# Kernel tuning notes

Measured on AMD Instinct MI355X. Metric: run time of the kernel, lower is better.

The kernel has to match this reference:

```python
import jax, jax.numpy as jnp
import numpy as np

E, T, D, H = 32, 65536, 512, 1024


def setup_inputs() -> dict:
    key = jax.random.key(0)
    k = jax.random.split(key, 7)
    norm = lambda kk, shp, sc: (jax.random.normal(kk, shp, jnp.float32) * sc)
    x = norm(k[0], (T, D), 1.0)
    w1 = norm(k[1], (E, D, H), D ** -0.5)   # per-expert up-proj (gate branch)
    b1 = norm(k[2], (E, H), 0.02)
    w3 = norm(k[3], (E, D, H), D ** -0.5)   # per-expert up-proj (linear branch)
    b3 = norm(k[4], (E, H), 0.02)
    w2 = norm(k[5], (E, H, D), H ** -0.5)   # per-expert down-proj
    b2 = norm(k[6], (E, D), 0.02)
    # tokens are pre-sorted by expert; uniform dispatch of T//E tokens per expert
    group_sizes = jnp.full((E,), T // E, jnp.int32)
    return dict(x=x, w1=w1, b1=b1, w3=w3, b3=b3, w2=w2, b2=b2,
                group_sizes=group_sizes)


def reference(x, w1, b1, w3, b3, w2, b2, group_sizes):
    # expert id per token, derived from contiguous group sizes
    bounds = jnp.cumsum(group_sizes)                       # [E]
    seg = jnp.searchsorted(bounds, jnp.arange(x.shape[0]), side='right')  # [T]
    # grouped GEMMs: per-expert weight bank applied to its contiguous token slab
    h1 = jax.lax.ragged_dot(x, w1, group_sizes) + b1[seg]  # [T,H]
    h3 = jax.lax.ragged_dot(x, w3, group_sizes) + b3[seg]  # [T,H]
    h = jax.nn.silu(h1) * h3                               # SwiGLU gate
    out = jax.lax.ragged_dot(h, w2, group_sizes) + b2[seg] # [T,D]
    return out
```

## Files before the change

kernel.cpp:

```cpp
#include <hip/hip_runtime.h>
#include <hip/hip_bf16.h>

#define TOK 65536
#define NE  32
#define DD  512
#define HH  1024
#define TPE 2048

typedef short s16x8  __attribute__((ext_vector_type(8)));
typedef float f32x16 __attribute__((ext_vector_type(16)));
using u16 = unsigned short;
using u32 = unsigned int;

__device__ __forceinline__ u16 f2bf(float f) {
  __bf16 h = (__bf16)f;
  return __builtin_bit_cast(u16, h);
}
__device__ __forceinline__ u32 pk2(float lo, float hi) {
  return (u32)f2bf(lo) | ((u32)f2bf(hi) << 16);
}
__device__ __forceinline__ int swz(int row, int colb) {
  return (row << 7) + (colb ^ ((row & 7) << 4));
}

#define MFMA(a, b, c) __builtin_amdgcn_mfma_f32_32x32x16_bf16(a, b, c, 0, 0, 0)
#define GLD(src, dst) __builtin_amdgcn_global_load_lds( \
    (const __attribute__((address_space(1))) void*)(src), \
    (__attribute__((address_space(3))) void*)(dst), 16, 0, 0)
#define SETP(n) __builtin_amdgcn_s_setprio(n)
#define SCHEDB() __builtin_amdgcn_sched_barrier(0)
#define SBAR()  __builtin_amdgcn_s_barrier()

__global__ __launch_bounds__(256) void p1_cvt_x(
    const float* __restrict__ x, u16* __restrict__ xb) {
  const size_t i = ((size_t)blockIdx.x * 256 + threadIdx.x) * 8;
  const float4 a = *(const float4*)(x + i);
  const float4 b = *(const float4*)(x + i + 4);
  uint4 v;
  v.x = pk2(a.x, a.y); v.y = pk2(a.z, a.w);
  v.z = pk2(b.x, b.y); v.w = pk2(b.z, b.w);
  *(uint4*)(xb + i) = v;
}

__global__ __launch_bounds__(256) void p2_w13t(
    const float* __restrict__ w1, const float* __restrict__ w3,
    u16* __restrict__ w13t) {
  __shared__ __align__(16) u16 L1[64 * 72], L3[64 * 72];
  const int bid = blockIdx.x;
  const int e = bid >> 7, rr = bid & 127;
  const int d0 = (rr & 7) << 6, h0 = (rr >> 3) << 6;
  const int t = threadIdx.x;
  const float* const s1 = w1 + (size_t)e * DD * HH + (size_t)d0 * HH + h0;
  const float* const s3 = w3 + (size_t)e * DD * HH + (size_t)d0 * HH + h0;
  const int cg = (t & 15) << 2, rbase = t >> 4;
#pragma unroll
  for (int j = 0; j < 4; ++j) {
    const int dr = rbase + (j << 4);
    const float4 a = *(const float4*)(s1 + (size_t)dr * HH + cg);
    const float4 b = *(const float4*)(s3 + (size_t)dr * HH + cg);
    L1[(cg + 0) * 72 + dr] = f2bf(a.x); L1[(cg + 1) * 72 + dr] = f2bf(a.y);
    L1[(cg + 2) * 72 + dr] = f2bf(a.z); L1[(cg + 3) * 72 + dr] = f2bf(a.w);
    L3[(cg + 0) * 72 + dr] = f2bf(b.x); L3[(cg + 1) * 72 + dr] = f2bf(b.y);
    L3[(cg + 2) * 72 + dr] = f2bf(b.z); L3[(cg + 3) * 72 + dr] = f2bf(b.w);
  }
  __syncthreads();
  u16* const dst = w13t + (size_t)e * (2 * HH) * DD;
  const int cb8 = (t & 7) << 3;
#pragma unroll
  for (int j = 0; j < 2; ++j) {
    const int nloc = (t >> 3) + (j << 5);
    const int n = h0 + nloc;
    const int R1 = ((n >> 5) << 6) + (n & 31);
    const uint4 v1 = *(const uint4*)(L1 + nloc * 72 + cb8);
    const uint4 v3 = *(const uint4*)(L3 + nloc * 72 + cb8);
    *(uint4*)(dst + (size_t)R1 * DD + d0 + cb8) = v1;
    *(uint4*)(dst + (size_t)(R1 + 32) * DD + d0 + cb8) = v3;
  }
}

__global__ __launch_bounds__(256) void p3_w2t(
    const float* __restrict__ w2, u16* __restrict__ w2t) {
  __shared__ __align__(16) u16 L[64 * 72];
  const int bid = blockIdx.x;
  const int e = bid >> 7, rr = bid & 127;
  const int d0 = (rr & 7) << 6, h0 = (rr >> 3) << 6;
  const int t = threadIdx.x;
  const float* const s = w2 + (size_t)e * HH * DD + (size_t)h0 * DD + d0;
  const int cg = (t & 15) << 2, rbase = t >> 4;
#pragma unroll
  for (int j = 0; j < 4; ++j) {
    const int hr = rbase + (j << 4);
    const float4 a = *(const float4*)(s + (size_t)hr * DD + cg);
    L[(cg + 0) * 72 + hr] = f2bf(a.x); L[(cg + 1) * 72 + hr] = f2bf(a.y);
    L[(cg + 2) * 72 + hr] = f2bf(a.z); L[(cg + 3) * 72 + hr] = f2bf(a.w);
  }
  __syncthreads();
  u16* const dst = w2t + (size_t)e * DD * HH;
  const int cb8 = (t & 7) << 3;
#pragma unroll
  for (int j = 0; j < 2; ++j) {
    const int dloc = (t >> 3) + (j << 5);
    const uint4 v = *(const uint4*)(L + dloc * 72 + cb8);
    *(uint4*)(dst + (size_t)(d0 + dloc) * HH + h0 + cb8) = v;
  }
}

template <int MODE>
__global__ __launch_bounds__(512, 2) void gemm4p(
    const u16* __restrict__ A, const u16* __restrict__ Bm,
    const float* __restrict__ bx, const float* __restrict__ by,
    void* __restrict__ outp) {
  constexpr int K  = MODE ? HH : DD;
  constexpr int NT = K >> 6;
  constexpr int NB = MODE ? 2 : 8;
  constexpr int NWG = NE * 8 * NB;
  __shared__ __align__(16) char lds[131072];

  int bid = blockIdx.x;
  bid = (bid & 7) * (NWG / 8) + (bid >> 3);
  const int e   = bid / (8 * NB);
  const int rr  = bid % (8 * NB);
  const int m_t = rr & 7;
  const int n_t = rr >> 3;
  const int rowbase = e * TPE + (m_t << 8);

  const int t = threadIdx.x;
  const int wv = t >> 6, lane = t & 63;
  const int l31 = lane & 31, half = lane >> 5;
  const int wm = wv >> 2, wn = wv & 3;

  const u16* const Abase = A + (size_t)rowbase * K;
  const u16* const Bbase = Bm + ((size_t)e * NB + n_t) * 256 * K;

  int srcoff0, srcoff1;
  {
    const int c0 = t,       lr0 = c0 >> 3, s0 = (c0 & 7) ^ (lr0 & 7);
    const int c1 = 512 + t, lr1 = c1 >> 3, s1 = (c1 & 7) ^ (lr1 & 7);
    srcoff0 = ((lr0 << 1) | (s0 >> 2)) * K + ((s0 & 3) << 3);
    srcoff1 = ((lr1 << 1) | (s1 >> 2)) * K + ((s1 & 3) << 3);
  }
  const int t16 = t << 4;

  auto stageQ = [&](int tau, int q) {
    const u16* const src = ((q & 1) ? Bbase : Abase) + tau * 64 + (q >> 1) * 32;
    char* const dst = lds + ((tau & 1) << 16) + (q << 14);
    GLD(src + srcoff0, dst + t16);
    GLD(src + srcoff1, dst + 8192 + t16);
  };

  const int lrow_off = l31 >> 1;
  const int pbit = l31 & 1;
  const int sw7 = lrow_off & 7;
  const int sA0 = (((pbit << 2) | 0 | half) ^ sw7) << 4;
  const int sA1 = (((pbit << 2) | 2 | half) ^ sw7) << 4;
  const int aoff = ((wm << 6) + lrow_off) << 7;
  const int boff = ((wn << 5) + lrow_off) << 7;

  f32x16 acc[4][2] = {};
  s16x8 b00{}, b01{}, b10{}, b11{};

#define VM6 asm volatile("s_waitcnt vmcnt(6)" ::: "memory")
#define VM4 asm volatile("s_waitcnt vmcnt(4)" ::: "memory")
#define VM0 asm volatile("s_waitcnt vmcnt(0)" ::: "memory")
#define NOPV ((void)0)

#define PHASE(T, KH, MH, DOB, STG, VM) do { \
  STG; VM; \
  SCHEDB(); SBAR(); SCHEDB(); \
  { const char* const Aq = lds + (((T) & 1) << 16) + ((KH) << 15); \
    const char* const Bq = Aq + 16384; \
    if (DOB) { \
      b00 = *(const s16x8*)(Bq + boff + 0 * 2048 + sA0); \
      b01 = *(const s16x8*)(Bq + boff + 1 * 2048 + sA0); \
      b10 = *(const s16x8*)(Bq + boff + 0 * 2048 + sA1); \
      b11 = *(const s16x8*)(Bq + boff + 1 * 2048 + sA1); \
    } \
    const s16x8 a0 = *(const s16x8*)(Aq + aoff + (2 * (MH)) * 2048 + sA0); \
    const s16x8 a1 = *(const s16x8*)(Aq + aoff + (2 * (MH)) * 2048 + sA1); \
    const s16x8 a2 = *(const s16x8*)(Aq + aoff + (2 * (MH) + 1) * 2048 + sA0); \
    const s16x8 a3 = *(const s16x8*)(Aq + aoff + (2 * (MH) + 1) * 2048 + sA1); \
    SETP(1); \
    acc[2 * (MH)][0]     = MFMA(a0, b00, acc[2 * (MH)][0]); \
    acc[2 * (MH)][1]     = MFMA(a0, b01, acc[2 * (MH)][1]); \
    acc[2 * (MH)][0]     = MFMA(a1, b10, acc[2 * (MH)][0]); \
    acc[2 * (MH)][1]     = MFMA(a1, b11, acc[2 * (MH)][1]); \
    acc[2 * (MH) + 1][0] = MFMA(a2, b00, acc[2 * (MH) + 1][0]); \
    acc[2 * (MH) + 1][1] = MFMA(a2, b01, acc[2 * (MH) + 1][1]); \
    acc[2 * (MH) + 1][0] = MFMA(a3, b10, acc[2 * (MH) + 1][0]); \
    acc[2 * (MH) + 1][1] = MFMA(a3, b11, acc[2 * (MH) + 1][1]); \
    SETP(0); \
  } \
} while (0)

  stageQ(0, 0); stageQ(0, 1); stageQ(0, 2); stageQ(0, 3);

#pragma unroll 2
  for (int kt = 0; kt < NT - 1; ++kt) {
    PHASE(kt, 0, 0, true,  stageQ(kt + 1, 0), VM6);
    PHASE(kt, 0, 1, false, stageQ(kt + 1, 1), NOPV);
    PHASE(kt, 1, 0, true,  stageQ(kt + 1, 2), VM6);
    PHASE(kt, 1, 1, false, stageQ(kt + 1, 3), NOPV);
  }
  PHASE(NT - 1, 0, 0, true,  NOPV, VM4);
  PHASE(NT - 1, 0, 1, false, NOPV, NOPV);
  PHASE(NT - 1, 1, 0, true,  NOPV, VM0);
  PHASE(NT - 1, 1, 1, false, NOPV, NOPV);

#undef PHASE
#undef VM6
#undef VM4
#undef VM0
#undef NOPV

  if constexpr (MODE == 0) {
    const int g = (n_t << 2) + wn;
    const int hcol = (g << 5) + l31;
    const float bv1 = bx[e * HH + hcol];
    const float bv3 = by[e * HH + hcol];
    u16* const hp = (u16*)outp;
#pragma unroll
    for (int mf = 0; mf < 4; ++mf) {
#pragma unroll
      for (int rg = 0; rg < 16; ++rg) {
        const int grow = rowbase + (wm << 7) + (mf << 5) +
                         (rg & 3) + ((rg >> 2) << 3) + (half << 2);
        const float s1 = acc[mf][0][rg] + bv1;
        const float s3 = acc[mf][1][rg] + bv3;
        hp[(size_t)grow * HH + hcol] = f2bf(s1 * s3 / (1.0f + __expf(-s1)));
      }
    }
  } else {
    float* const op = (float*)outp;
#pragma unroll
    for (int mf = 0; mf < 4; ++mf) {
#pragma unroll
      for (int nf = 0; nf < 2; ++nf) {
        const int col = (n_t << 8) + (wn << 6) + (nf << 5) + l31;
        const float bv = bx[e * DD + col];
#pragma unroll
        for (int rg = 0; rg < 16; ++rg) {
          const int grow = rowbase + (wm << 7) + (mf << 5) +
                           (rg & 3) + ((rg >> 2) << 3) + (half << 2);
          op[(size_t)grow * DD + col] = acc[mf][nf][rg] + bv;
        }
      }
    }
  }
}

__global__ __launch_bounds__(256, 2) void k1_up_swiglu(
    const float* __restrict__ x,  const float* __restrict__ w1,
    const float* __restrict__ b1, const float* __restrict__ w3,
    const float* __restrict__ b3, u16* __restrict__ hbuf) {
  __shared__ __align__(16) char lds[32768];
  char* const As  = lds;
  char* const B1s = lds + 16384;
  char* const B3s = lds + 24576;
  const int bid = blockIdx.x;
  const int e = bid >> 8, rr = bid & 255;
  const int m_t = rr & 15, n_t = rr >> 4;
  const int rowbase = e * TPE + (m_t << 7), colbase = n_t << 6;
  const int t = threadIdx.x, wv = t >> 6, lane = t & 63;
  const int l31 = lane & 31, half = lane >> 5;
  const int wm = wv >> 1, wn = wv & 1;
  const int ag = t & 15, am0 = t >> 4, bn = t & 63, bk0 = t >> 6;
  const float* const xb = x + (size_t)rowbase * DD + (ag << 2);
  const size_t woff = (size_t)e * (DD * HH) + colbase + bn;
  const float* const w1b = w1 + woff;
  const float* const w3b = w3 + woff;
  float4 ra[8]; float rb1[16], rb3[16];
  auto gload = [&](int kt) {
    const float* xp = xb + (kt << 6);
#pragma unroll
    for (int j = 0; j < 8; ++j)
      ra[j] = *(const float4*)(xp + (size_t)(am0 + (j << 4)) * DD);
#pragma unroll
    for (int j = 0; j < 2; ++j) {
      const int k0 = (kt << 6) + ((bk0 + (j << 2)) << 3);
#pragma unroll
      for (int i = 0; i < 8; ++i) {
        rb1[(j << 3) + i] = w1b[(size_t)(k0 + i) * HH];
        rb3[(j << 3) + i] = w3b[(size_t)(k0 + i) * HH];
      }
    }
  };
  f32x16 acc10 = {}, acc11 = {}, acc30 = {}, acc31 = {};
  gload(0);
  for (int kt = 0; kt < 8; ++kt) {
    if (kt) __syncthreads();
#pragma unroll
    for (int j = 0; j < 8; ++j) {
      const int m = am0 + (j << 4);
      uint2 v; v.x = pk2(ra[j].x, ra[j].y); v.y = pk2(ra[j].z, ra[j].w);
      *(uint2*)(As + swz(m, ag << 3)) = v;
    }
#pragma unroll
    for (int j = 0; j < 2; ++j) {
      const int kg = bk0 + (j << 2);
      uint4 v;
      v.x = pk2(rb1[(j << 3) + 0], rb1[(j << 3) + 1]);
      v.y = pk2(rb1[(j << 3) + 2], rb1[(j << 3) + 3]);
      v.z = pk2(rb1[(j << 3) + 4], rb1[(j << 3) + 5]);
      v.w = pk2(rb1[(j << 3) + 6], rb1[(j << 3) + 7]);
      *(uint4*)(B1s + swz(bn, kg << 4)) = v;
      v.x = pk2(rb3[(j << 3) + 0], rb3[(j << 3) + 1]);
      v.y = pk2(rb3[(j << 3) + 2], rb3[(j << 3) + 3]);
      v.z = pk2(rb3[(j << 3) + 4], rb3[(j << 3) + 5]);
      v.w = pk2(rb3[(j << 3) + 6], rb3[(j << 3) + 7]);
      *(uint4*)(B3s + swz(bn, kg << 4)) = v;
    }
    __syncthreads();
    if (kt < 7) gload(kt + 1);
#pragma unroll
    for (int kk = 0; kk < 4; ++kk) {
      const int colb = (kk << 5) + (half << 4);
      const s16x8 a0 = *(const s16x8*)(As  + swz((wm << 6) + l31,      colb));
      const s16x8 a1 = *(const s16x8*)(As  + swz((wm << 6) + 32 + l31, colb));
      const s16x8 f1 = *(const s16x8*)(B1s + swz((wn << 5) + l31,      colb));
      const s16x8 f3 = *(const s16x8*)(B3s + swz((wn << 5) + l31,      colb));
      acc10 = MFMA(a0, f1, acc10); acc30 = MFMA(a0, f3, acc30);
      acc11 = MFMA(a1, f1, acc11); acc31 = MFMA(a1, f3, acc31);
    }
  }
  const int gcol = colbase + (wn << 5) + l31;
  const float bv1 = b1[e * HH + gcol], bv3 = b3[e * HH + gcol];
  u16* const hp = hbuf + gcol;
#pragma unroll
  for (int mb = 0; mb < 2; ++mb) {
    const f32x16 A1 = mb ? acc11 : acc10;
    const f32x16 A3 = mb ? acc31 : acc30;
#pragma unroll
    for (int rg = 0; rg < 16; ++rg) {
      const int grow = rowbase + (wm << 6) + (mb << 5) +
                       (rg & 3) + ((rg >> 2) << 3) + (half << 2);
      const float s1 = A1[rg] + bv1, s3 = A3[rg] + bv3;
      hp[(size_t)grow * HH] = f2bf(s1 * s3 / (1.0f + __expf(-s1)));
    }
  }
}

__global__ __launch_bounds__(256, 2) void k2_down(
    const u16* __restrict__ hbuf, const float* __restrict__ w2,
    const float* __restrict__ b2, float* __restrict__ out) {
  __shared__ __align__(16) char lds[32768];
  char* const As = lds;
  char* const Bs = lds + 16384;
  const int bid = blockIdx.x;
  const int e = bid >> 6, rr = bid & 63;
  const int m_t = rr & 15, n_t = rr >> 4;
  const int rowbase = e * TPE + (m_t << 7), colbase = n_t << 7;
  const int t = threadIdx.x, wv = t >> 6, lane = t & 63;
  const int l31 = lane & 31, half = lane >> 5;
  const int wm = wv >> 1, wn = wv & 1;
  const int ag = t & 7, am0 = t >> 3, bnn = t & 127, bk0 = t >> 7;
  const u16* const hb = hbuf + (size_t)rowbase * HH + (ag << 3);
  const float* const w2b = w2 + (size_t)e * (HH * DD) + colbase + bnn;
  uint4 ra[4]; float rb[32];
  auto gload = [&](int kt) {
#pragma unroll
    for (int j = 0; j < 4; ++j)
      ra[j] = *(const uint4*)(hb + (size_t)(am0 + (j << 5)) * HH + (kt << 6));
#pragma unroll
    for (int j = 0; j < 4; ++j) {
      const int k0 = (kt << 6) + ((bk0 + (j << 1)) << 3);
#pragma unroll
      for (int i = 0; i < 8; ++i)
        rb[(j << 3) + i] = w2b[(size_t)(k0 + i) * DD];
    }
  };
  f32x16 c00 = {}, c01 = {}, c10 = {}, c11 = {};
  gload(0);
  for (int kt = 0; kt < 16; ++kt) {
    if (kt) __syncthreads();
#pragma unroll
    for (int j = 0; j < 4; ++j)
      *(uint4*)(As + swz(am0 + (j << 5), ag << 4)) = ra[j];
#pragma unroll
    for (int j = 0; j < 4; ++j) {
      const int kg = bk0 + (j << 1);
      uint4 v;
      v.x = pk2(rb[(j << 3) + 0], rb[(j << 3) + 1]);
      v.y = pk2(rb[(j << 3) + 2], rb[(j << 3) + 3]);
      v.z = pk2(rb[(j << 3) + 4], rb[(j << 3) + 5]);
      v.w = pk2(rb[(j << 3) + 6], rb[(j << 3) + 7]);
      *(uint4*)(Bs + swz(bnn, kg << 4)) = v;
    }
    __syncthreads();
    if (kt < 15) gload(kt + 1);
#pragma unroll
    for (int kk = 0; kk < 4; ++kk) {
      const int colb = (kk << 5) + (half << 4);
      const s16x8 af0 = *(const s16x8*)(As + swz((wm << 6) + l31,      colb));
      const s16x8 af1 = *(const s16x8*)(As + swz((wm << 6) + 32 + l31, colb));
      const s16x8 bf0 = *(const s16x8*)(Bs + swz((wn << 6) + l31,      colb));
      const s16x8 bf1 = *(const s16x8*)(Bs + swz((wn << 6) + 32 + l31, colb));
      c00 = MFMA(af0, bf0, c00); c01 = MFMA(af0, bf1, c01);
      c10 = MFMA(af1, bf0, c10); c11 = MFMA(af1, bf1, c11);
    }
  }
#pragma unroll
  for (int mb = 0; mb < 2; ++mb) {
#pragma unroll
    for (int nb = 0; nb < 2; ++nb) {
      const f32x16 c = mb ? (nb ? c11 : c10) : (nb ? c01 : c00);
      const int gcol = colbase + (wn << 6) + (nb << 5) + l31;
      const float bv = b2[e * DD + gcol];
#pragma unroll
      for (int rg = 0; rg < 16; ++rg) {
        const int grow = rowbase + (wm << 6) + (mb << 5) +
                         (rg & 3) + ((rg >> 2) << 3) + (half << 2);
        out[(size_t)grow * DD + gcol] = c[rg] + bv;
      }
    }
  }
}

extern "C" void kernel_launch(void* const* d_in, const int* in_sizes, int n_in,
                              void* d_out, int out_size, void* d_ws, size_t ws_size,
                              hipStream_t stream) {
  const float* x  = (const float*)d_in[0];
  const float* w1 = (const float*)d_in[1];
  const float* b1 = (const float*)d_in[2];
  const float* w3 = (const float*)d_in[3];
  const float* b3 = (const float*)d_in[4];
  const float* w2 = (const float*)d_in[5];
  const float* b2 = (const float*)d_in[6];

  const size_t W13T_B = (size_t)NE * 2 * HH * DD * 2;
  const size_t W2T_B  = (size_t)NE * DD * HH * 2;
  const size_t H_B    = (size_t)TOK * HH * 2;

  if (ws_size >= W13T_B + W2T_B + H_B) {
    u16* const xb   = (u16*)d_out;
    u16* const w13t = (u16*)d_ws;
    u16* const w2t  = (u16*)((char*)d_ws + W13T_B);
    u16* const hbuf = (u16*)((char*)d_ws + W13T_B + W2T_B);

    p1_cvt_x<<<dim3(TOK * DD / 2048), dim3(256), 0, stream>>>(x, xb);
    p2_w13t <<<dim3(NE * 128),        dim3(256), 0, stream>>>(w1, w3, w13t);
    p3_w2t  <<<dim3(NE * 128),        dim3(256), 0, stream>>>(w2, w2t);
    gemm4p<0><<<dim3(NE * 64), dim3(512), 0, stream>>>(xb, w13t, b1, b3, hbuf);
    gemm4p<1><<<dim3(NE * 16), dim3(512), 0, stream>>>(hbuf, w2t, b2, nullptr, d_out);
  } else {
    u16* hbuf = (ws_size >= H_B) ? (u16*)d_ws : (u16*)d_out;
    k1_up_swiglu<<<dim3(NE * 256), dim3(256), 0, stream>>>(x, w1, b1, w3, b3, hbuf);
    k2_down<<<dim3(NE * 64), dim3(256), 0, stream>>>(hbuf, w2, b2, (float*)d_out);
  }
}
```

Before: 360.5 us.

## Reorder GEMM pipeline to issue LDS fragment reads before the barrier

Each phase of the main GEMM loop now issues its LDS fragment loads first, then the global-to-LDS staging and the vmcnt wait. After the barrier it waits on lgkmcnt(0) and runs the MFMAs. Staging is regrouped into two half-stage bursts per k-tile with vmcnt(4) waits, a prologue wait and barrier are added, and the loop is no longer unrolled by 2. The aim is to overlap LDS read latency with barrier and global-load waits. The tighter lgkm waits could expose latency differently and must keep the double-buffer ordering correct.

```diff
diff --git a/kernel.cpp b/kernel.cpp
--- a/kernel.cpp
+++ b/kernel.cpp
@@ -106,7 +106,7 @@
 }
 
 template <int MODE>
-__global__ __launch_bounds__(512, 2) void gemm4p(
+__global__ __launch_bounds__(512, 2) void gemm4s(
     const u16* __restrict__ A, const u16* __restrict__ Bm,
     const float* __restrict__ bx, const float* __restrict__ by,
     void* __restrict__ outp) {
@@ -159,57 +159,60 @@
   f32x16 acc[4][2] = {};
   s16x8 b00{}, b01{}, b10{}, b11{};
 
-#define VM6 asm volatile("s_waitcnt vmcnt(6)" ::: "memory")
 #define VM4 asm volatile("s_waitcnt vmcnt(4)" ::: "memory")
 #define VM0 asm volatile("s_waitcnt vmcnt(0)" ::: "memory")
+#define LGKM0 asm volatile("s_waitcnt lgkmcnt(0)" ::: "memory")
 #define NOPV ((void)0)
 
-#define PHASE(T, KH, MH, DOB, STG, VM) do { \
+#define PHASE(CB, KH, MH, DOB, STG, VM) do { \
+  const char* const Aq = (CB) + ((KH) << 15); \
+  const char* const Bq = Aq + 16384; \
+  if (DOB) { \
+    b00 = *(const s16x8*)(Bq + boff + 0 * 2048 + sA0); \
+    b01 = *(const s16x8*)(Bq + boff + 1 * 2048 + sA0); \
+    b10 = *(const s16x8*)(Bq + boff + 0 * 2048 + sA1); \
+    b11 = *(const s16x8*)(Bq + boff + 1 * 2048 + sA1); \
+  } \
+  const s16x8 a0 = *(const s16x8*)(Aq + aoff + (2 * (MH)) * 2048 + sA0); \
+  const s16x8 a1 = *(const s16x8*)(Aq + aoff + (2 * (MH)) * 2048 + sA1); \
+  const s16x8 a2 = *(const s16x8*)(Aq + aoff + (2 * (MH) + 1) * 2048 + sA0); \
+  const s16x8 a3 = *(const s16x8*)(Aq + aoff + (2 * (MH) + 1) * 2048 + sA1); \
   STG; VM; \
-  SCHEDB(); SBAR(); SCHEDB(); \
-  { const char* const Aq = lds + (((T) & 1) << 16) + ((KH) << 15); \
-    const char* const Bq = Aq + 16384; \
-    if (DOB) { \
-      b00 = *(const s16x8*)(Bq + boff + 0 * 2048 + sA0); \
-      b01 = *(const s16x8*)(Bq + boff + 1 * 2048 + sA0); \
-      b10 = *(const s16x8*)(Bq + boff + 0 * 2048 + sA1); \
-      b11 = *(const s16x8*)(Bq + boff + 1 * 2048 + sA1); \
-    } \
-    const s16x8 a0 = *(const s16x8*)(Aq + aoff + (2 * (MH)) * 2048 + sA0); \
-    const s16x8 a1 = *(const s16x8*)(Aq + aoff + (2 * (MH)) * 2048 + sA1); \
-    const s16x8 a2 = *(const s16x8*)(Aq + aoff + (2 * (MH) + 1) * 2048 + sA0); \
-    const s16x8 a3 = *(const s16x8*)(Aq + aoff + (2 * (MH) + 1) * 2048 + sA1); \
-    SETP(1); \
-    acc[2 * (MH)][0]     = MFMA(a0, b00, acc[2 * (MH)][0]); \
-    acc[2 * (MH)][1]     = MFMA(a0, b01, acc[2 * (MH)][1]); \
-    acc[2 * (MH)][0]     = MFMA(a1, b10, acc[2 * (MH)][0]); \
-    acc[2 * (MH)][1]     = MFMA(a1, b11, acc[2 * (MH)][1]); \
-    acc[2 * (MH) + 1][0] = MFMA(a2, b00, acc[2 * (MH) + 1][0]); \
-    acc[2 * (MH) + 1][1] = MFMA(a2, b01, acc[2 * (MH) + 1][1]); \
-    acc[2 * (MH) + 1][0] = MFMA(a3, b10, acc[2 * (MH) + 1][0]); \
-    acc[2 * (MH) + 1][1] = MFMA(a3, b11, acc[2 * (MH) + 1][1]); \
-    SETP(0); \
-  } \
+  SCHEDB(); SBAR(); LGKM0; SCHEDB(); \
+  SETP(1); \
+  acc[2 * (MH)][0]     = MFMA(a0, b00, acc[2 * (MH)][0]); \
+  acc[2 * (MH)][1]     = MFMA(a0, b01, acc[2 * (MH)][1]); \
+  acc[2 * (MH)][0]     = MFMA(a1, b10, acc[2 * (MH)][0]); \
+  acc[2 * (MH)][1]     = MFMA(a1, b11, acc[2 * (MH)][1]); \
+  acc[2 * (MH) + 1][0] = MFMA(a2, b00, acc[2 * (MH) + 1][0]); \
+  acc[2 * (MH) + 1][1] = MFMA(a2, b01, acc[2 * (MH) + 1][1]); \
+  acc[2 * (MH) + 1][0] = MFMA(a3, b10, acc[2 * (MH) + 1][0]); \
+  acc[2 * (MH) + 1][1] = MFMA(a3, b11, acc[2 * (MH) + 1][1]); \
+  SETP(0); \
 } while (0)
 
   stageQ(0, 0); stageQ(0, 1); stageQ(0, 2); stageQ(0, 3);
-
-#pragma unroll 2
+  VM4; SCHEDB(); SBAR();
+
   for (int kt = 0; kt < NT - 1; ++kt) {
-    PHASE(kt, 0, 0, true,  stageQ(kt + 1, 0), VM6);
-    PHASE(kt, 0, 1, false, stageQ(kt + 1, 1), NOPV);
-    PHASE(kt, 1, 0, true,  stageQ(kt + 1, 2), VM6);
-    PHASE(kt, 1, 1, false, stageQ(kt + 1, 3), NOPV);
-  }
-  PHASE(NT - 1, 0, 0, true,  NOPV, VM4);
-  PHASE(NT - 1, 0, 1, false, NOPV, NOPV);
-  PHASE(NT - 1, 1, 0, true,  NOPV, VM0);
-  PHASE(NT - 1, 1, 1, false, NOPV, NOPV);
+    const char* const cb = lds + ((kt & 1) << 16);
+    PHASE(cb, 0, 0, true,  (stageQ(kt + 1, 0), stageQ(kt + 1, 1)), NOPV);
+    PHASE(cb, 0, 1, false, NOPV, VM4);
+    PHASE(cb, 1, 0, true,  (stageQ(kt + 1, 2), stageQ(kt + 1, 3)), NOPV);
+    PHASE(cb, 1, 1, false, NOPV, VM4);
+  }
+  {
+    const char* const cb = lds + (((NT - 1) & 1) << 16);
+    PHASE(cb, 0, 0, true,  NOPV, NOPV);
+    PHASE(cb, 0, 1, false, NOPV, VM0);
+    PHASE(cb, 1, 0, true,  NOPV, NOPV);
+    PHASE(cb, 1, 1, false, NOPV, NOPV);
+  }
 
 #undef PHASE
-#undef VM6
 #undef VM4
 #undef VM0
+#undef LGKM0
 #undef NOPV
 
   if constexpr (MODE == 0) {
@@ -439,8 +442,8 @@
     p1_cvt_x<<<dim3(TOK * DD / 2048), dim3(256), 0, stream>>>(x, xb);
     p2_w13t <<<dim3(NE * 128),        dim3(256), 0, stream>>>(w1, w3, w13t);
     p3_w2t  <<<dim3(NE * 128),        dim3(256), 0, stream>>>(w2, w2t);
-    gemm4p<0><<<dim3(NE * 64), dim3(512), 0, stream>>>(xb, w13t, b1, b3, hbuf);
-    gemm4p<1><<<dim3(NE * 16), dim3(512), 0, stream>>>(hbuf, w2t, b2, nullptr, d_out);
+    gemm4s<0><<<dim3(NE * 64), dim3(512), 0, stream>>>(xb, w13t, b1, b3, hbuf);
+    gemm4s<1><<<dim3(NE * 16), dim3(512), 0, stream>>>(hbuf, w2t, b2, nullptr, d_out);
   } else {
     u16* hbuf = (ws_size >= H_B) ? (u16*)d_ws : (u16*)d_out;
     k1_up_swiglu<<<dim3(NE * 256), dim3(256), 0, stream>>>(x, w1, b1, w3, b3, hbuf);
```

Result: no change. 366.3 us (+1.6%).
